# Kernel optimization log

Hardware: AMD Instinct MI355X
Metric: run time of the kernel (lower is better)

The kernel has to match this reference:

```python
import jax, jax.numpy as jnp
import numpy as np

# --- static problem geometry (compile-time constants, as in MinkowskiEngine decompositions) ---
N_TOTAL = 500000          # total points across all clouds
C = 128                   # feature channels
G = 32                    # GroupNorm groups
EPS = 1e-5                # torch GroupNorm default
LENGTHS = np.array([40000, 55000, 70000, 45000, 80000, 65000, 90000, 55000])  # points per cloud
assert LENGTHS.sum() == N_TOTAL
B = len(LENGTHS)
SEG = np.repeat(np.arange(B), LENGTHS)  # [N] cloud id for each position of the concatenated permutation


def setup_inputs() -> dict:
    key = jax.random.key(0)
    k1, k2, k3, k4 = jax.random.split(key, 4)
    feats = jax.random.normal(k1, (N_TOTAL, C), dtype=jnp.float32)   # x.F
    # concatenated decomposition_permutations: a permutation of arange(N)
    perm = jax.random.permutation(k2, N_TOTAL).astype(jnp.int64)
    gamma = 1.0 + 0.1 * jax.random.normal(k3, (C,), dtype=jnp.float32)  # GroupNorm weight
    beta = 0.1 * jax.random.normal(k4, (C,), dtype=jnp.float32)         # GroupNorm bias
    return {"feats": feats, "gamma": gamma, "beta": beta, "perm": perm}


def reference(feats, gamma, beta, perm):
    Cg = C // G
    seg = jnp.asarray(SEG)                              # [N]
    x = feats[perm]                                     # [N, C] per-cloud gather (concatenated)
    xg = x.reshape(-1, G, Cg)                           # [N, G, Cg]
    # per-(cloud, group) statistics over all points of the cloud and channels of the group
    s = jax.ops.segment_sum(xg.sum(-1), seg, num_segments=B)            # [B, G]
    ss = jax.ops.segment_sum((xg * xg).sum(-1), seg, num_segments=B)    # [B, G]
    cnt = jnp.asarray(LENGTHS * Cg, dtype=feats.dtype)[:, None]          # [B, 1]
    mean = s / cnt
    var = ss / cnt - mean * mean
    inv = jax.lax.rsqrt(var + EPS)                      # [B, G]
    xn = (xg - mean[seg][:, :, None]) * inv[seg][:, :, None]             # [N, G, Cg]
    y = xn.reshape(-1, C) * gamma + beta                # [N, C] affine per channel
    # scatter back via inverse permutation: out[perm[i]] = y[i]
    out = jnp.zeros_like(y).at[perm].set(y)
    return out
```

## Files before the change

kernel.cpp:

```cpp
#include <hip/hip_runtime.h>

#define N_TOTAL 500000
#define C 128
#define G 32
#define CG 4
#define NB 8
#define EPS 1e-5f

__device__ __forceinline__ int cloud_of(int i) {
    int c = 0;
    c += (i >= 40000);
    c += (i >= 95000);
    c += (i >= 165000);
    c += (i >= 210000);
    c += (i >= 290000);
    c += (i >= 355000);
    c += (i >= 445000);
    return c;
}

__device__ const float d_cnt[NB] = {160000.f, 220000.f, 280000.f, 180000.f,
                                    320000.f, 260000.f, 360000.f, 220000.f};

__global__ void gn_zero(float* __restrict__ ws) {
    int i = threadIdx.x;
    if (i < 2 * NB * G) ws[i] = 0.f;
}

__global__ __launch_bounds__(256) void gn_stats(const float* __restrict__ feats,
                                                const int* __restrict__ perm,
                                                float* __restrict__ ws,
                                                int rows_per_block) {
    __shared__ float lacc[2 * NB * G];
    int tid = threadIdx.x;
    for (int idx = tid; idx < 2 * NB * G; idx += 256) lacc[idx] = 0.f;
    __syncthreads();

    const int g = tid & 31;
    const int rsub = tid >> 5;
    int start = blockIdx.x * rows_per_block;
    int end = start + rows_per_block;
    if (end > N_TOTAL) end = N_TOTAL;

    float s = 0.f, ss = 0.f;
    int cur = -1;
    for (int row = start + rsub; row < end; row += 8) {
        int cl = cloud_of(row);
        if (cl != cur) {
            if (cur >= 0 && (s != 0.f || ss != 0.f)) {
                atomicAdd(&lacc[cur * G + g], s);
                atomicAdd(&lacc[NB * G + cur * G + g], ss);
            }
            cur = cl; s = 0.f; ss = 0.f;
        }
        int p = perm[row];
        const float4* rp = (const float4*)(feats + ((long long)p << 7));
        float4 v = rp[g];
        s  += v.x + v.y + v.z + v.w;
        ss += v.x * v.x + v.y * v.y + v.z * v.z + v.w * v.w;
    }
    if (cur >= 0 && (s != 0.f || ss != 0.f)) {
        atomicAdd(&lacc[cur * G + g], s);
        atomicAdd(&lacc[NB * G + cur * G + g], ss);
    }
    __syncthreads();

    for (int idx = tid; idx < 2 * NB * G; idx += 256) {
        float a = lacc[idx];
        if (a != 0.f) atomicAdd(&ws[idx], a);
    }
}

__global__ __launch_bounds__(256) void gn_apply(const float* __restrict__ feats,
                                                const float* __restrict__ gamma,
                                                const float* __restrict__ beta,
                                                const int* __restrict__ perm,
                                                const float* __restrict__ ws,
                                                float* __restrict__ out) {
    __shared__ float lmean[NB * G];
    __shared__ float linv[NB * G];
    int tid = threadIdx.x;
    for (int idx = tid; idx < NB * G; idx += 256) {
        float s = ws[idx];
        float ss = ws[NB * G + idx];
        float cnt = d_cnt[idx >> 5];
        float m = s / cnt;
        float var = ss / cnt - m * m;
        lmean[idx] = m;
        linv[idx] = rsqrtf(var + EPS);
    }
    __syncthreads();

    const int g = tid & 31;
    const int rsub = tid >> 5;
    float4 gm = ((const float4*)gamma)[g];
    float4 bt = ((const float4*)beta)[g];

    int stride = gridDim.x * 8;
    for (int row = blockIdx.x * 8 + rsub; row < N_TOTAL; row += stride) {
        int cl = cloud_of(row);
        int p = perm[row];
        const float4* rp = (const float4*)(feats + ((long long)p << 7));
        float4 v = rp[g];
        float m = lmean[cl * G + g];
        float inv = linv[cl * G + g];
        float4 y;
        y.x = (v.x - m) * inv * gm.x + bt.x;
        y.y = (v.y - m) * inv * gm.y + bt.y;
        y.z = (v.z - m) * inv * gm.z + bt.z;
        y.w = (v.w - m) * inv * gm.w + bt.w;
        ((float4*)(out + ((long long)p << 7)))[g] = y;
    }
}

extern "C" void kernel_launch(void* const* d_in, const int* in_sizes, int n_in,
                              void* d_out, int out_size, void* d_ws, size_t ws_size,
                              hipStream_t stream) {
    const float* feats = (const float*)d_in[0];
    const float* gamma = (const float*)d_in[1];
    const float* beta  = (const float*)d_in[2];
    const int*   perm  = (const int*)d_in[3];
    float* out = (float*)d_out;
    float* ws  = (float*)d_ws;

    gn_zero<<<1, 512, 0, stream>>>(ws);

    const int nblk = 2048;
    int rpb = (N_TOTAL + nblk - 1) / nblk;
    gn_stats<<<nblk, 256, 0, stream>>>(feats, perm, ws, rpb);
    gn_apply<<<nblk, 256, 0, stream>>>(feats, gamma, beta, perm, ws, out);
}
```

Baseline: 162.8 us.

## Scatter per-point cloud ids once and stream features in natural order

A prep kernel writes a byte cloud id for every original point index by scattering through the permutation, and also zeroes the accumulators. The stats and apply kernels then read features and write outputs sequentially in row order instead of gathering and scattering through perm. This removes the random 512-byte row accesses from both passes. Stats now keep per-cloud register accumulators selected by a predicated loop, and outputs use nontemporal stores. The cost is an extra scattered byte write pass and more registers per thread.

```diff
diff --git a/kernel.cpp b/kernel.cpp
--- a/kernel.cpp
+++ b/kernel.cpp
@@ -3,9 +3,11 @@
 #define N_TOTAL 500000
 #define C 128
 #define G 32
-#define CG 4
 #define NB 8
 #define EPS 1e-5f
+#define NBLK 2048
+
+typedef float f4 __attribute__((ext_vector_type(4)));
 
 __device__ __forceinline__ int cloud_of(int i) {
     int c = 0;
@@ -22,18 +24,24 @@
 __device__ const float d_cnt[NB] = {160000.f, 220000.f, 280000.f, 180000.f,
                                     320000.f, 260000.f, 360000.f, 220000.f};
 
-__global__ void gn_zero(float* __restrict__ ws) {
-    int i = threadIdx.x;
-    if (i < 2 * NB * G) ws[i] = 0.f;
+
+__global__ __launch_bounds__(256) void gn_prep(const int* __restrict__ perm,
+                                               unsigned char* __restrict__ cid,
+                                               float* __restrict__ ws) {
+    int gid = blockIdx.x * 256 + threadIdx.x;
+    if (gid < 2 * NB * G) ws[gid] = 0.f;
+    int stride = gridDim.x * 256;
+    for (int i = gid; i < N_TOTAL; i += stride)
+        cid[perm[i]] = (unsigned char)cloud_of(i);
 }
 
 __global__ __launch_bounds__(256) void gn_stats(const float* __restrict__ feats,
-                                                const int* __restrict__ perm,
+                                                const unsigned char* __restrict__ cid,
                                                 float* __restrict__ ws,
                                                 int rows_per_block) {
     __shared__ float lacc[2 * NB * G];
     int tid = threadIdx.x;
-    for (int idx = tid; idx < 2 * NB * G; idx += 256) lacc[idx] = 0.f;
+    for (int k = tid; k < 2 * NB * G; k += 256) lacc[k] = 0.f;
     __syncthreads();
 
     const int g = tid & 31;
@@ -42,74 +50,76 @@
     int end = start + rows_per_block;
     if (end > N_TOTAL) end = N_TOTAL;
 
-    float s = 0.f, ss = 0.f;
-    int cur = -1;
+    float s[NB], ss[NB];
+#pragma unroll
+    for (int b = 0; b < NB; b++) { s[b] = 0.f; ss[b] = 0.f; }
+
     for (int row = start + rsub; row < end; row += 8) {
-        int cl = cloud_of(row);
-        if (cl != cur) {
-            if (cur >= 0 && (s != 0.f || ss != 0.f)) {
-                atomicAdd(&lacc[cur * G + g], s);
-                atomicAdd(&lacc[NB * G + cur * G + g], ss);
-            }
-            cur = cl; s = 0.f; ss = 0.f;
+        int cl = cid[row];
+        f4 v = ((const f4*)(feats + ((long long)row << 7)))[g];
+        float rs = v.x + v.y + v.z + v.w;
+        float rss = v.x * v.x + v.y * v.y + v.z * v.z + v.w * v.w;
+#pragma unroll
+        for (int b = 0; b < NB; b++) {
+            if (cl == b) { s[b] += rs; ss[b] += rss; }
         }
-        int p = perm[row];
-        const float4* rp = (const float4*)(feats + ((long long)p << 7));
-        float4 v = rp[g];
-        s  += v.x + v.y + v.z + v.w;
-        ss += v.x * v.x + v.y * v.y + v.z * v.z + v.w * v.w;
     }
-    if (cur >= 0 && (s != 0.f || ss != 0.f)) {
-        atomicAdd(&lacc[cur * G + g], s);
-        atomicAdd(&lacc[NB * G + cur * G + g], ss);
+#pragma unroll
+    for (int b = 0; b < NB; b++) {
+        if (s[b] != 0.f || ss[b] != 0.f) {
+            atomicAdd(&lacc[b * G + g], s[b]);
+            atomicAdd(&lacc[NB * G + b * G + g], ss[b]);
+        }
     }
     __syncthreads();
 
-    for (int idx = tid; idx < 2 * NB * G; idx += 256) {
-        float a = lacc[idx];
-        if (a != 0.f) atomicAdd(&ws[idx], a);
+    for (int k = tid; k < 2 * NB * G; k += 256) {
+        float a = lacc[k];
+        if (a != 0.f) atomicAdd(&ws[k], a);
     }
 }
 
 __global__ __launch_bounds__(256) void gn_apply(const float* __restrict__ feats,
+                                                const unsigned char* __restrict__ cid,
                                                 const float* __restrict__ gamma,
                                                 const float* __restrict__ beta,
-                                                const int* __restrict__ perm,
                                                 const float* __restrict__ ws,
-                                                float* __restrict__ out) {
+                                                float* __restrict__ out,
+                                                int rows_per_block) {
     __shared__ float lmean[NB * G];
     __shared__ float linv[NB * G];
     int tid = threadIdx.x;
-    for (int idx = tid; idx < NB * G; idx += 256) {
-        float s = ws[idx];
-        float ss = ws[NB * G + idx];
-        float cnt = d_cnt[idx >> 5];
-        float m = s / cnt;
-        float var = ss / cnt - m * m;
-        lmean[idx] = m;
-        linv[idx] = rsqrtf(var + EPS);
+    {
+        float sm = ws[tid];
+        float sq = ws[NB * G + tid];
+        float cnt = d_cnt[tid >> 5];
+        float m = sm / cnt;
+        float var = sq / cnt - m * m;
+        lmean[tid] = m;
+        linv[tid] = rsqrtf(var + EPS);
     }
     __syncthreads();
 
     const int g = tid & 31;
     const int rsub = tid >> 5;
-    float4 gm = ((const float4*)gamma)[g];
-    float4 bt = ((const float4*)beta)[g];
+    f4 gm = ((const f4*)gamma)[g];
+    f4 bt = ((const f4*)beta)[g];
 
-    int stride = gridDim.x * 8;
-    for (int row = blockIdx.x * 8 + rsub; row < N_TOTAL; row += stride) {
-        int cl = cloud_of(row);
-        int p = perm[row];
-        const float4* rp = (const float4*)(feats + ((long long)p << 7));
-        float4 v = rp[g];
+    int start = blockIdx.x * rows_per_block;
+    int end = start + rows_per_block;
+    if (end > N_TOTAL) end = N_TOTAL;
+
+    for (int row = start + rsub; row < end; row += 8) {
+        int cl = cid[row];
+        f4 v = ((const f4*)(feats + ((long long)row << 7)))[g];
         float m = lmean[cl * G + g];
         float inv = linv[cl * G + g];
-        float4 y;
+        f4 y;
         y.x = (v.x - m) * inv * gm.x + bt.x;
         y.y = (v.y - m) * inv * gm.y + bt.y;
         y.z = (v.z - m) * inv * gm.z + bt.z;
         y.w = (v.w - m) * inv * gm.w + bt.w;
-        ((float4*)(out + ((long long)p << 7)))[g] = y;
+        __builtin_nontemporal_store(y, (f4*)(out + ((long long)row << 7)) + g);
     }
 }
 
@@ -122,11 +132,11 @@
     const int*   perm  = (const int*)d_in[3];
     float* out = (float*)d_out;
     float* ws  = (float*)d_ws;
+    unsigned char* cid = (unsigned char*)d_ws + 4096;
 
-    gn_zero<<<1, 512, 0, stream>>>(ws);
+    gn_prep<<<512, 256, 0, stream>>>(perm, cid, ws);
 
-    const int nblk = 2048;
-    int rpb = (N_TOTAL + nblk - 1) / nblk;
-    gn_stats<<<nblk, 256, 0, stream>>>(feats, perm, ws, rpb);
-    gn_apply<<<nblk, 256, 0, stream>>>(feats, gamma, beta, perm, ws, out);
+    int rpb = (N_TOTAL + NBLK - 1) / NBLK;
+    gn_stats<<<NBLK, 256, 0, stream>>>(feats, cid, ws, rpb);
+    gn_apply<<<NBLK, 256, 0, stream>>>(feats, cid, gamma, beta, ws, out, rpb);
 }
```

After: 171.2 us. +5.1%, slower.

## Split stats and apply into per-cloud chunk launches interleaved for cache reuse

Applied to the files above, without the earlier changes.

Replaces the two whole-array passes with per-cloud kernels: stats for cloud k is launched, then apply for cloud k-1, so the gathered rows of a cloud are re-read while still likely resident in the last-level cache. Cloud id computation is removed since each launch covers one cloud, and outputs are written with nontemporal stores. In exchange it adds many more kernel launches with small per-launch work, and each 2048-block grid has only a few rows per block.

```diff
diff --git a/kernel.cpp b/kernel.cpp
--- a/kernel.cpp
+++ b/kernel.cpp
@@ -3,113 +3,87 @@
 #define N_TOTAL 500000
 #define C 128
 #define G 32
-#define CG 4
 #define NB 8
 #define EPS 1e-5f
+#define NBLK 2048
 
-__device__ __forceinline__ int cloud_of(int i) {
-    int c = 0;
-    c += (i >= 40000);
-    c += (i >= 95000);
-    c += (i >= 165000);
-    c += (i >= 210000);
-    c += (i >= 290000);
-    c += (i >= 355000);
-    c += (i >= 445000);
-    return c;
-}
+typedef float f4 __attribute__((ext_vector_type(4)));
 
-__device__ const float d_cnt[NB] = {160000.f, 220000.f, 280000.f, 180000.f,
-                                    320000.f, 260000.f, 360000.f, 220000.f};
 
 __global__ void gn_zero(float* __restrict__ ws) {
     int i = threadIdx.x;
     if (i < 2 * NB * G) ws[i] = 0.f;
 }
 
-__global__ __launch_bounds__(256) void gn_stats(const float* __restrict__ feats,
-                                                const int* __restrict__ perm,
-                                                float* __restrict__ ws,
-                                                int rows_per_block) {
-    __shared__ float lacc[2 * NB * G];
+__global__ __launch_bounds__(256) void gn_stats_chunk(const float* __restrict__ feats,
+                                                      const int* __restrict__ perm,
+                                                      float* __restrict__ ws,
+                                                      int i_begin, int i_end, int cloud) {
+    __shared__ float lacc[2 * G];
     int tid = threadIdx.x;
-    for (int idx = tid; idx < 2 * NB * G; idx += 256) lacc[idx] = 0.f;
+    if (tid < 2 * G) lacc[tid] = 0.f;
     __syncthreads();
 
     const int g = tid & 31;
     const int rsub = tid >> 5;
-    int start = blockIdx.x * rows_per_block;
-    int end = start + rows_per_block;
-    if (end > N_TOTAL) end = N_TOTAL;
-
     float s = 0.f, ss = 0.f;
-    int cur = -1;
-    for (int row = start + rsub; row < end; row += 8) {
-        int cl = cloud_of(row);
-        if (cl != cur) {
-            if (cur >= 0 && (s != 0.f || ss != 0.f)) {
-                atomicAdd(&lacc[cur * G + g], s);
-                atomicAdd(&lacc[NB * G + cur * G + g], ss);
-            }
-            cur = cl; s = 0.f; ss = 0.f;
-        }
-        int p = perm[row];
-        const float4* rp = (const float4*)(feats + ((long long)p << 7));
-        float4 v = rp[g];
+    for (int i = i_begin + blockIdx.x * 8 + rsub; i < i_end; i += NBLK * 8) {
+        int p = perm[i];
+        f4 v = ((const f4*)(feats + ((long long)p << 7)))[g];
         s  += v.x + v.y + v.z + v.w;
         ss += v.x * v.x + v.y * v.y + v.z * v.z + v.w * v.w;
     }
-    if (cur >= 0 && (s != 0.f || ss != 0.f)) {
-        atomicAdd(&lacc[cur * G + g], s);
-        atomicAdd(&lacc[NB * G + cur * G + g], ss);
-    }
+    atomicAdd(&lacc[g], s);
+    atomicAdd(&lacc[G + g], ss);
     __syncthreads();
 
-    for (int idx = tid; idx < 2 * NB * G; idx += 256) {
-        float a = lacc[idx];
-        if (a != 0.f) atomicAdd(&ws[idx], a);
+    if (tid < 2 * G) {
+        float a = lacc[tid];
+        if (a != 0.f) {
+            float* dst = (tid < G) ? &ws[cloud * G + tid]
+                                   : &ws[NB * G + cloud * G + (tid - G)];
+            atomicAdd(dst, a);
+        }
     }
 }
 
-__global__ __launch_bounds__(256) void gn_apply(const float* __restrict__ feats,
-                                                const float* __restrict__ gamma,
-                                                const float* __restrict__ beta,
-                                                const int* __restrict__ perm,
-                                                const float* __restrict__ ws,
-                                                float* __restrict__ out) {
-    __shared__ float lmean[NB * G];
-    __shared__ float linv[NB * G];
+__global__ __launch_bounds__(256) void gn_apply_chunk(const float* __restrict__ feats,
+                                                      const int* __restrict__ perm,
+                                                      const float* __restrict__ gamma,
+                                                      const float* __restrict__ beta,
+                                                      const float* __restrict__ ws,
+                                                      float* __restrict__ out,
+                                                      int i_begin, int i_end,
+                                                      float inv_cnt, int cloud) {
+    __shared__ float lmean[G];
+    __shared__ float linv[G];
     int tid = threadIdx.x;
-    for (int idx = tid; idx < NB * G; idx += 256) {
-        float s = ws[idx];
-        float ss = ws[NB * G + idx];
-        float cnt = d_cnt[idx >> 5];
-        float m = s / cnt;
-        float var = ss / cnt - m * m;
-        lmean[idx] = m;
-        linv[idx] = rsqrtf(var + EPS);
+    if (tid < G) {
+        float sm = ws[cloud * G + tid];
+        float sq = ws[NB * G + cloud * G + tid];
+        float m = sm * inv_cnt;
+        float var = sq * inv_cnt - m * m;
+        lmean[tid] = m;
+        linv[tid] = rsqrtf(var + EPS);
     }
     __syncthreads();
 
     const int g = tid & 31;
     const int rsub = tid >> 5;
-    float4 gm = ((const float4*)gamma)[g];
-    float4 bt = ((const float4*)beta)[g];
+    float m = lmean[g];
+    float inv = linv[g];
+    f4 gm = ((const f4*)gamma)[g];
+    f4 bt = ((const f4*)beta)[g];
 
-    int stride = gridDim.x * 8;
-    for (int row = blockIdx.x * 8 + rsub; row < N_TOTAL; row += stride) {
-        int cl = cloud_of(row);
-        int p = perm[row];
-        const float4* rp = (const float4*)(feats + ((long long)p << 7));
-        float4 v = rp[g];
-        float m = lmean[cl * G + g];
-        float inv = linv[cl * G + g];
-        float4 y;
+    for (int i = i_begin + blockIdx.x * 8 + rsub; i < i_end; i += NBLK * 8) {
+        int p = perm[i];
+        f4 v = ((const f4*)(feats + ((long long)p << 7)))[g];
+        f4 y;
         y.x = (v.x - m) * inv * gm.x + bt.x;
         y.y = (v.y - m) * inv * gm.y + bt.y;
         y.z = (v.z - m) * inv * gm.z + bt.z;
         y.w = (v.w - m) * inv * gm.w + bt.w;
-        ((float4*)(out + ((long long)p << 7)))[g] = y;
+        __builtin_nontemporal_store(y, (f4*)(out + ((long long)p << 7)) + g);
     }
 }
 
@@ -123,10 +97,25 @@
     float* out = (float*)d_out;
     float* ws  = (float*)d_ws;
 
+    static const int bounds[NB + 1] = {0, 40000, 95000, 165000, 210000,
+                                       290000, 355000, 445000, 500000};
+    static const float inv_cnt[NB] = {1.f / 160000.f, 1.f / 220000.f,
+                                      1.f / 280000.f, 1.f / 180000.f,
+                                      1.f / 320000.f, 1.f / 260000.f,
+                                      1.f / 360000.f, 1.f / 220000.f};
+
     gn_zero<<<1, 512, 0, stream>>>(ws);
 
-    const int nblk = 2048;
-    int rpb = (N_TOTAL + nblk - 1) / nblk;
-    gn_stats<<<nblk, 256, 0, stream>>>(feats, perm, ws, rpb);
-    gn_apply<<<nblk, 256, 0, stream>>>(feats, gamma, beta, perm, ws, out);
+    gn_stats_chunk<<<NBLK, 256, 0, stream>>>(feats, perm, ws,
+                                             bounds[0], bounds[1], 0);
+    for (int k = 1; k < NB; ++k) {
+        gn_stats_chunk<<<NBLK, 256, 0, stream>>>(feats, perm, ws,
+                                                 bounds[k], bounds[k + 1], k);
+        gn_apply_chunk<<<NBLK, 256, 0, stream>>>(feats, perm, gamma, beta, ws, out,
+                                                 bounds[k - 1], bounds[k],
+                                                 inv_cnt[k - 1], k - 1);
+    }
+    gn_apply_chunk<<<NBLK, 256, 0, stream>>>(feats, perm, gamma, beta, ws, out,
+                                             bounds[NB - 1], bounds[NB],
+                                             inv_cnt[NB - 1], NB - 1);
 }
```

Result: slower. 372.7 us (+128.9%).
